# Kernel optimization log

Hardware: AMD Instinct MI355X
Metric: run time of the kernel (lower is better)

## Reference

```python
import jax, jax.numpy as jnp
import numpy as np

D_MODEL = 2048
NUM_HEADS = 16
D_FF = 8192
BATCH = 4
SEQ = 2048


def setup_inputs() -> dict:
    key = jax.random.key(0)
    ks = jax.random.split(key, 16)
    s_attn = 1.0 / np.sqrt(D_MODEL)
    s_ff1 = 1.0 / np.sqrt(D_MODEL)
    s_ff2 = 1.0 / np.sqrt(D_FF)
    return {
        "x": jax.random.normal(ks[0], (BATCH, SEQ, D_MODEL), dtype=jnp.float32),
        "Wq": jax.random.normal(ks[1], (D_MODEL, D_MODEL), dtype=jnp.float32) * s_attn,
        "bq": jnp.zeros((D_MODEL,), dtype=jnp.float32),
        "Wk": jax.random.normal(ks[2], (D_MODEL, D_MODEL), dtype=jnp.float32) * s_attn,
        "bk": jnp.zeros((D_MODEL,), dtype=jnp.float32),
        "Wv": jax.random.normal(ks[3], (D_MODEL, D_MODEL), dtype=jnp.float32) * s_attn,
        "bv": jnp.zeros((D_MODEL,), dtype=jnp.float32),
        "Wo": jax.random.normal(ks[4], (D_MODEL, D_MODEL), dtype=jnp.float32) * s_attn,
        "bo": jnp.zeros((D_MODEL,), dtype=jnp.float32),
        "W1": jax.random.normal(ks[5], (D_MODEL, D_FF), dtype=jnp.float32) * s_ff1,
        "b1": jnp.zeros((D_FF,), dtype=jnp.float32),
        "W2": jax.random.normal(ks[6], (D_FF, D_MODEL), dtype=jnp.float32) * s_ff2,
        "b2": jnp.zeros((D_MODEL,), dtype=jnp.float32),
        "ln1_g": jnp.ones((D_MODEL,), dtype=jnp.float32),
        "ln1_b": jnp.zeros((D_MODEL,), dtype=jnp.float32),
        "ln2_g": jnp.ones((D_MODEL,), dtype=jnp.float32),
        "ln2_b": jnp.zeros((D_MODEL,), dtype=jnp.float32),
    }


def _layer_norm(x, g, b, eps=1e-5):
    mu = jnp.mean(x, axis=-1, keepdims=True)
    var = jnp.mean(jnp.square(x - mu), axis=-1, keepdims=True)
    return (x - mu) * jax.lax.rsqrt(var + eps) * g + b


def _attention(h, Wq, bq, Wk, bk, Wv, bv, Wo, bo):
    B, S, D = h.shape
    H = NUM_HEADS
    dk = D // H
    q = (h @ Wq + bq).reshape(B, S, H, dk).transpose(0, 2, 1, 3)  # bhsd
    k = (h @ Wk + bk).reshape(B, S, H, dk).transpose(0, 2, 1, 3)
    v = (h @ Wv + bv).reshape(B, S, H, dk).transpose(0, 2, 1, 3)
    logits = jnp.einsum("bhqd,bhkd->bhqk", q, k) / jnp.sqrt(jnp.float32(dk))
    causal = jnp.triu(jnp.ones((S, S), dtype=bool), k=1)  # True above diagonal
    logits = jnp.where(causal, -jnp.inf, logits)
    attn = jax.nn.softmax(logits, axis=-1)
    out = jnp.einsum("bhqk,bhkd->bhqd", attn, v)
    out = out.transpose(0, 2, 1, 3).reshape(B, S, D)
    return out @ Wo + bo


def reference(x, Wq, bq, Wk, bk, Wv, bv, Wo, bo, W1, b1, W2, b2,
              ln1_g, ln1_b, ln2_g, ln2_b):
    # Pre-LN attention block + residual
    h = _layer_norm(x, ln1_g, ln1_b)
    x = x + _attention(h, Wq, bq, Wk, bk, Wv, bv, Wo, bo)
    # Pre-LN FFN block + residual (GELU activation)
    h = _layer_norm(x, ln2_g, ln2_b)
    ff = jax.nn.gelu(h @ W1 + b1, approximate=False) @ W2 + b2
    return x + ff
```

## Files before the change

kernel.cpp:

```cpp
#include <hip/hip_runtime.h>
#include <hip/hip_bf16.h>

#define D_MODEL 2048
#define NUM_HEADS 16
#define D_FF 8192
#define BATCH 4
#define SEQ 2048
#define DK 128
#define MTOT (BATCH * SEQ)

typedef __attribute__((ext_vector_type(8))) short short8;
typedef __attribute__((ext_vector_type(4))) short short4v;
typedef __attribute__((ext_vector_type(4))) float f32x4;

#define MFMA16(a, b, c) __builtin_amdgcn_mfma_f32_16x16x32_bf16(a, b, c, 0, 0, 0)

#define GLOAD16(gp, lp)                                                        \
  __builtin_amdgcn_global_load_lds(                                            \
      (const __attribute__((address_space(1))) void*)(gp),                     \
      (__attribute__((address_space(3))) void*)(lp), 16, 0, 0)

static __device__ __forceinline__ unsigned short f2bf(float f) {
  return __builtin_bit_cast(unsigned short, __float2bfloat16(f));
}

__global__ __launch_bounds__(256) void transpose_cvt_kernel(
    const float* __restrict__ in, __hip_bfloat16* __restrict__ out, int K, int N) {
  __shared__ float tile[32][33];
  const int n0 = blockIdx.x * 32, k0 = blockIdx.y * 32;
  const int tx = threadIdx.x & 31, ty = threadIdx.x >> 5;
#pragma unroll
  for (int i = 0; i < 4; ++i)
    tile[ty + i * 8][tx] = in[(size_t)(k0 + ty + i * 8) * N + n0 + tx];
  __syncthreads();
#pragma unroll
  for (int i = 0; i < 4; ++i)
    out[(size_t)(n0 + ty + i * 8) * K + k0 + tx] = __float2bfloat16(tile[tx][ty + i * 8]);
}

__global__ __launch_bounds__(256) void layernorm_kernel(
    const float* __restrict__ x, const float* __restrict__ g,
    const float* __restrict__ bta, __hip_bfloat16* __restrict__ out) {
  const int row = blockIdx.x;
  const int tid = threadIdx.x;
  const float* xr = x + (size_t)row * D_MODEL;
  float4 v0 = *(const float4*)(xr + tid * 8);
  float4 v1 = *(const float4*)(xr + tid * 8 + 4);
  float s = v0.x + v0.y + v0.z + v0.w + v1.x + v1.y + v1.z + v1.w;
  float q = v0.x * v0.x + v0.y * v0.y + v0.z * v0.z + v0.w * v0.w +
            v1.x * v1.x + v1.y * v1.y + v1.z * v1.z + v1.w * v1.w;
#pragma unroll
  for (int off = 1; off < 64; off <<= 1) {
    s += __shfl_xor(s, off);
    q += __shfl_xor(q, off);
  }
  __shared__ float rs[4], rq[4];
  if ((tid & 63) == 0) {
    rs[tid >> 6] = s;
    rq[tid >> 6] = q;
  }
  __syncthreads();
  s = rs[0] + rs[1] + rs[2] + rs[3];
  q = rq[0] + rq[1] + rq[2] + rq[3];
  const float mu = s * (1.0f / D_MODEL);
  const float var = q * (1.0f / D_MODEL) - mu * mu;
  const float rstd = rsqrtf(var + 1e-5f);
  float4 g0 = *(const float4*)(g + tid * 8);
  float4 g1 = *(const float4*)(g + tid * 8 + 4);
  float4 b0 = *(const float4*)(bta + tid * 8);
  float4 b1 = *(const float4*)(bta + tid * 8 + 4);
  short8 o;
  o[0] = (short)f2bf((v0.x - mu) * rstd * g0.x + b0.x);
  o[1] = (short)f2bf((v0.y - mu) * rstd * g0.y + b0.y);
  o[2] = (short)f2bf((v0.z - mu) * rstd * g0.z + b0.z);
  o[3] = (short)f2bf((v0.w - mu) * rstd * g0.w + b0.w);
  o[4] = (short)f2bf((v1.x - mu) * rstd * g1.x + b1.x);
  o[5] = (short)f2bf((v1.y - mu) * rstd * g1.y + b1.y);
  o[6] = (short)f2bf((v1.z - mu) * rstd * g1.z + b1.z);
  o[7] = (short)f2bf((v1.w - mu) * rstd * g1.w + b1.w);
  *(short8*)(out + (size_t)row * D_MODEL + tid * 8) = o;
}

enum { EPI_BF16 = 0, EPI_VT = 1, EPI_RESID = 2, EPI_GELU = 3 };

template <int EPI>
__global__ __launch_bounds__(256, 2) void gemm_kernel(
    const __hip_bfloat16* __restrict__ A, const __hip_bfloat16* __restrict__ Bt,
    const float* __restrict__ bias, const float* __restrict__ resid,
    void* __restrict__ outv, int M, int N, int K) {
  __shared__ __align__(16) unsigned char sA[16384];
  __shared__ __align__(16) unsigned char sB[16384];
  const int tid = threadIdx.x;
  const int lane = tid & 63, w = tid >> 6;
  const int l15 = lane & 15, lg = lane >> 4;
  const int m0 = blockIdx.y * 128, n0 = blockIdx.x * 128;
  const int wm = (w >> 1) * 64, wn = (w & 1) * 64;

  f32x4 acc[4][4] = {};

  const int row8 = lane >> 3;
  const int g8 = (lane & 7) ^ row8;

  for (int kt = 0; kt < K; kt += 64) {
#pragma unroll
    for (int i = 0; i < 4; ++i) {
      const int c = w * 4 + i;
      const int row = c * 8 + row8;
      GLOAD16(A + (size_t)(m0 + row) * K + kt + g8 * 8, sA + c * 1024);
      GLOAD16(Bt + (size_t)(n0 + row) * K + kt + g8 * 8, sB + c * 1024);
    }
    __syncthreads();
#pragma unroll
    for (int ks = 0; ks < 2; ++ks) {
      const int cb = ks * 4 + lg;
      short8 af[4], bf[4];
#pragma unroll
      for (int f = 0; f < 4; ++f) {
        const int ra = wm + f * 16 + l15;
        af[f] = *(const short8*)(sA + ra * 128 + ((cb ^ (ra & 7)) << 4));
        const int rb = wn + f * 16 + l15;
        bf[f] = *(const short8*)(sB + rb * 128 + ((cb ^ (rb & 7)) << 4));
      }
#pragma unroll
      for (int fi = 0; fi < 4; ++fi)
#pragma unroll
        for (int fj = 0; fj < 4; ++fj)
          acc[fi][fj] = MFMA16(af[fi], bf[fj], acc[fi][fj]);
    }
    __syncthreads();
  }

#pragma unroll
  for (int fi = 0; fi < 4; ++fi) {
#pragma unroll
    for (int fj = 0; fj < 4; ++fj) {
      const int mb = m0 + wm + fi * 16 + lg * 4;
      const int n = n0 + wn + fj * 16 + l15;
      const float bv = bias ? bias[n] : 0.0f;
      if constexpr (EPI == EPI_VT) {
        const int bb = mb >> 11, ss = mb & (SEQ - 1);
        const int hh = n >> 7, dd = n & (DK - 1);
        short4v pk;
#pragma unroll
        for (int r = 0; r < 4; ++r) pk[r] = (short)f2bf(acc[fi][fj][r] + bv);
        __hip_bfloat16* o = (__hip_bfloat16*)outv;
        *(short4v*)(o + ((size_t)((bb * NUM_HEADS + hh) * DK + dd)) * SEQ + ss) = pk;
      } else {
#pragma unroll
        for (int r = 0; r < 4; ++r) {
          const int m = mb + r;
          const float v = acc[fi][fj][r] + bv;
          if constexpr (EPI == EPI_BF16) {
            ((__hip_bfloat16*)outv)[(size_t)m * N + n] = __float2bfloat16(v);
          } else if constexpr (EPI == EPI_GELU) {
            const float ge = 0.5f * v * (1.0f + erff(v * 0.70710678118654752f));
            ((__hip_bfloat16*)outv)[(size_t)m * N + n] = __float2bfloat16(ge);
          } else {
            ((float*)outv)[(size_t)m * N + n] = resid[(size_t)m * N + n] + v;
          }
        }
      }
    }
  }
}

__global__ __launch_bounds__(512, 4) void attn_kernel(
    const __hip_bfloat16* __restrict__ Qm, const __hip_bfloat16* __restrict__ Km,
    const __hip_bfloat16* __restrict__ Vt, __hip_bfloat16* __restrict__ Om) {
  __shared__ __align__(16) unsigned char Kl[2][16384];
  __shared__ __align__(16) unsigned char Vl[2][16384];
  __shared__ __align__(16) unsigned char Pl[16384];
  const int tid = threadIdx.x;
  const int lane = tid & 63, w = tid >> 6;
  const int l15 = lane & 15, lg = lane >> 4;
  const int bh = blockIdx.y, b = bh >> 4, h = bh & 15;
  const int q0 = blockIdx.x * 128;
  const int qw = q0 + w * 16;
  const int row8 = lane >> 3;
  const int nt = (q0 >> 6) + 2;

  short8 qf[4];
  const __hip_bfloat16* qbase = Qm + (size_t)(b * SEQ + qw + l15) * D_MODEL + h * DK;
#pragma unroll
  for (int ks = 0; ks < 4; ++ks) qf[ks] = *(const short8*)(qbase + ks * 32 + lg * 8);

  float m_run[4], l_run[4];
  f32x4 acc_o[8];
#pragma unroll
  for (int r = 0; r < 4; ++r) { m_run[r] = -1e30f; l_run[r] = 0.0f; }
#pragma unroll
  for (int fd = 0; fd < 8; ++fd) acc_o[fd] = (f32x4){0.f, 0.f, 0.f, 0.f};

  auto STAGE = [&](int tt) {
    unsigned char* kb = Kl[tt & 1];
    unsigned char* vb = Vl[tt & 1];
    const int t0 = tt * 64;
#pragma unroll
    for (int i = 0; i < 2; ++i) {
      const int c = w * 2 + i;
      const int row = c * 4 + lg;
      const int gcb = l15 ^ (row & 7);
      GLOAD16(Km + (size_t)(b * SEQ + t0 + row) * D_MODEL + h * DK + gcb * 8,
              kb + c * 1024);
    }
#pragma unroll
    for (int i = 0; i < 2; ++i) {
      const int c = w * 2 + i;
      const int row = c * 8 + row8;
      const int gcb = (lane & 7) ^ (row & 7);
      GLOAD16(Vt + (size_t)(bh * DK + row) * SEQ + t0 + gcb * 8, vb + c * 1024);
    }
  };

  STAGE(0);
  for (int t = 0; t < nt; ++t) {
    const int t0 = t * 64;
    if (t + 1 < nt) {
      STAGE(t + 1);
      asm volatile("s_waitcnt vmcnt(4)" ::: "memory");
    } else {
      asm volatile("s_waitcnt vmcnt(0)" ::: "memory");
    }
    __builtin_amdgcn_s_barrier();
    asm volatile("" ::: "memory");
    if (t0 <= qw + 15) {
      const unsigned char* kb = Kl[t & 1];
      const unsigned char* vb = Vl[t & 1];
      f32x4 sacc[4];
#pragma unroll
      for (int fn = 0; fn < 4; ++fn) sacc[fn] = (f32x4){0.f, 0.f, 0.f, 0.f};
#pragma unroll
      for (int ks = 0; ks < 4; ++ks) {
        const int cb = ks * 4 + lg;
#pragma unroll
        for (int fn = 0; fn < 4; ++fn) {
          const int rn = fn * 16 + l15;
          short8 kf = *(const short8*)(kb + rn * 256 + ((cb ^ (rn & 7)) << 4));
          sacc[fn] = MFMA16(qf[ks], kf, sacc[fn]);
        }
      }
      const float scale = 0.088388347648318447f;
      float mt[4] = {-1e30f, -1e30f, -1e30f, -1e30f};
#pragma unroll
      for (int fn = 0; fn < 4; ++fn) {
        const int key = t0 + fn * 16 + l15;
#pragma unroll
        for (int r = 0; r < 4; ++r) {
          const int qg = qw + lg * 4 + r;
          float sv = sacc[fn][r] * scale;
          sv = (key <= qg) ? sv : -1e30f;
          sacc[fn][r] = sv;
          mt[r] = fmaxf(mt[r], sv);
        }
      }
      float alpha[4], ls[4];
#pragma unroll
      for (int r = 0; r < 4; ++r) {
#pragma unroll
        for (int off = 1; off < 16; off <<= 1) mt[r] = fmaxf(mt[r], __shfl_xor(mt[r], off));
        const float mnew = fmaxf(m_run[r], mt[r]);
        alpha[r] = __expf(m_run[r] - mnew);
        m_run[r] = mnew;
        ls[r] = 0.0f;
      }
#pragma unroll
      for (int fn = 0; fn < 4; ++fn)
#pragma unroll
        for (int r = 0; r < 4; ++r) {
          const float p = __expf(sacc[fn][r] - m_run[r]);
          sacc[fn][r] = p;
          ls[r] += p;
        }
#pragma unroll
      for (int r = 0; r < 4; ++r) {
#pragma unroll
        for (int off = 1; off < 16; off <<= 1) ls[r] += __shfl_xor(ls[r], off);
        l_run[r] = l_run[r] * alpha[r] + ls[r];
      }
#pragma unroll
      for (int fd = 0; fd < 8; ++fd)
#pragma unroll
        for (int r = 0; r < 4; ++r) acc_o[fd][r] *= alpha[r];
      unsigned char* pw = Pl + w * 2048;
#pragma unroll
      for (int fn = 0; fn < 4; ++fn) {
        const int tt = fn * 16 + l15;
#pragma unroll
        for (int r = 0; r < 4; ++r) {
          const int qq = lg * 4 + r;
          *(unsigned short*)(pw + qq * 128 + (((tt >> 3) ^ (qq & 7)) << 4) +
                             (tt & 7) * 2) = f2bf(sacc[fn][r]);
        }
      }
#pragma unroll
      for (int ks = 0; ks < 2; ++ks) {
#pragma unroll
        for (int half = 0; half < 2; ++half) {
          const int tb = (ks * 2 + half) * 2 + (lg & 1) + (lg >> 1) * 0;
        }
        const int tb = ks * 4 + lg;
        short8 pf = *(const short8*)(Pl + w * 2048 + l15 * 128 +
                                     ((tb ^ (l15 & 7)) << 4));
        const int cb = ks * 4 + lg;
#pragma unroll
        for (int fd = 0; fd < 8; ++fd) {
          const int rv = fd * 16 + l15;
          short8 vf = *(const short8*)(vb + rv * 128 + ((cb ^ (rv & 7)) << 4));
          acc_o[fd] = MFMA16(pf, vf, acc_o[fd]);
        }
      }
    }
    asm volatile("" ::: "memory");
    __builtin_amdgcn_s_barrier();
    asm volatile("" ::: "memory");
  }
#pragma unroll
  for (int r = 0; r < 4; ++r) {
    const float inv = 1.0f / l_run[r];
    const int qg = qw + lg * 4 + r;
    __hip_bfloat16* ob = Om + (size_t)(b * SEQ + qg) * D_MODEL + h * DK + l15;
#pragma unroll
    for (int fd = 0; fd < 8; ++fd)
      ob[fd * 16] = __float2bfloat16(acc_o[fd][r] * inv);
  }
}

extern "C" void kernel_launch(void* const* d_in, const int* in_sizes, int n_in,
                              void* d_out, int out_size, void* d_ws, size_t ws_size,
                              hipStream_t stream) {
  (void)in_sizes; (void)n_in; (void)out_size;
  const size_t MB = 1024 * 1024;
  if (ws_size < 192 * MB) return;

  const float* x  = (const float*)d_in[0];
  const float* Wq = (const float*)d_in[1];
  const float* bq = (const float*)d_in[2];
  const float* Wk = (const float*)d_in[3];
  const float* bk = (const float*)d_in[4];
  const float* Wv = (const float*)d_in[5];
  const float* bv = (const float*)d_in[6];
  const float* Wo = (const float*)d_in[7];
  const float* bo = (const float*)d_in[8];
  const float* W1 = (const float*)d_in[9];
  const float* b1 = (const float*)d_in[10];
  const float* W2 = (const float*)d_in[11];
  const float* b2 = (const float*)d_in[12];
  const float* g1 = (const float*)d_in[13];
  const float* be1 = (const float*)d_in[14];
  const float* g2 = (const float*)d_in[15];
  const float* be2 = (const float*)d_in[16];

  char* ws = (char*)d_ws;
  __hip_bfloat16* Hb  = (__hip_bfloat16*)(ws + 0 * MB);
  __hip_bfloat16* Qb  = (__hip_bfloat16*)(ws + 32 * MB);
  __hip_bfloat16* Kb  = (__hip_bfloat16*)(ws + 64 * MB);
  __hip_bfloat16* Vtb = (__hip_bfloat16*)(ws + 96 * MB);
  __hip_bfloat16* AOb = (__hip_bfloat16*)(ws + 128 * MB);
  __hip_bfloat16* W1T = (__hip_bfloat16*)(ws + 32 * MB);
  __hip_bfloat16* W2T = (__hip_bfloat16*)(ws + 64 * MB);
  __hip_bfloat16* FF1 = (__hip_bfloat16*)(ws + 96 * MB);
  __hip_bfloat16* WqT = (__hip_bfloat16*)(ws + 160 * MB);
  __hip_bfloat16* WkT = (__hip_bfloat16*)(ws + 168 * MB);
  __hip_bfloat16* WvT = (__hip_bfloat16*)(ws + 176 * MB);
  __hip_bfloat16* WoT = (__hip_bfloat16*)(ws + 184 * MB);
  float* X2 = (float*)d_out;

  const dim3 tb(256);
  transpose_cvt_kernel<<<dim3(64, 64), tb, 0, stream>>>(Wq, WqT, 2048, 2048);
  transpose_cvt_kernel<<<dim3(64, 64), tb, 0, stream>>>(Wk, WkT, 2048, 2048);
  transpose_cvt_kernel<<<dim3(64, 64), tb, 0, stream>>>(Wv, WvT, 2048, 2048);
  transpose_cvt_kernel<<<dim3(64, 64), tb, 0, stream>>>(Wo, WoT, 2048, 2048);

  layernorm_kernel<<<MTOT, tb, 0, stream>>>(x, g1, be1, Hb);

  const dim3 gQKV(2048 / 128, MTOT / 128);
  gemm_kernel<EPI_BF16><<<gQKV, tb, 0, stream>>>(Hb, WqT, bq, nullptr, Qb, MTOT, 2048, 2048);
  gemm_kernel<EPI_BF16><<<gQKV, tb, 0, stream>>>(Hb, WkT, bk, nullptr, Kb, MTOT, 2048, 2048);
  gemm_kernel<EPI_VT><<<gQKV, tb, 0, stream>>>(Hb, WvT, bv, nullptr, Vtb, MTOT, 2048, 2048);

  attn_kernel<<<dim3(SEQ / 128, BATCH * NUM_HEADS), dim3(512), 0, stream>>>(Qb, Kb, Vtb, AOb);

  transpose_cvt_kernel<<<dim3(256, 64), tb, 0, stream>>>(W1, W1T, 2048, 8192);
  transpose_cvt_kernel<<<dim3(64, 256), tb, 0, stream>>>(W2, W2T, 8192, 2048);

  gemm_kernel<EPI_RESID><<<gQKV, tb, 0, stream>>>(AOb, WoT, bo, x, X2, MTOT, 2048, 2048);

  layernorm_kernel<<<MTOT, tb, 0, stream>>>(X2, g2, be2, Hb);

  for (int c = 0; c < 2; ++c) {
    const size_t moff = (size_t)c * 4096;
    gemm_kernel<EPI_GELU><<<dim3(8192 / 128, 4096 / 128), tb, 0, stream>>>(
        Hb + moff * D_MODEL, W1T, b1, nullptr, FF1, 4096, 8192, 2048);
    gemm_kernel<EPI_RESID><<<dim3(2048 / 128, 4096 / 128), tb, 0, stream>>>(
        FF1, W2T, b2, X2 + moff * D_MODEL, X2 + moff * D_MODEL, 4096, 2048, 8192);
  }
}
```

Baseline: 1.376 ms.

## Triple-buffer GEMM K-loop with 256x128 tiles and 512-thread blocks

The bf16 GEMM moves from a 128x128 tile with 256 threads and two barriers per K-step to a 256x128 tile with 8 waves. It now uses a three-stage LDS ring filled by global_load_lds, issued two K-steps ahead and gated by vmcnt waits and one barrier per step. MFMA blocks are wrapped in s_setprio to favour the math waves. The goal is to hide global-load latency behind MFMA work and to raise data reuse per block. The cost is 144KB of LDS per block, which limits occupancy to one block per CU, and fewer blocks for the smaller GEMMs.

After: 1.348 ms. -2.0%, faster.

```diff
diff --git a/kernel.cpp b/kernel.cpp
--- a/kernel.cpp
+++ b/kernel.cpp
@@ -84,16 +84,15 @@
 enum { EPI_BF16 = 0, EPI_VT = 1, EPI_RESID = 2, EPI_GELU = 3 };
 
 template <int EPI>
-__global__ __launch_bounds__(256, 2) void gemm_kernel(
+__global__ __launch_bounds__(512, 2) void gemm_kernel(
     const __hip_bfloat16* __restrict__ A, const __hip_bfloat16* __restrict__ Bt,
     const float* __restrict__ bias, const float* __restrict__ resid,
     void* __restrict__ outv, int M, int N, int K) {
-  __shared__ __align__(16) unsigned char sA[16384];
-  __shared__ __align__(16) unsigned char sB[16384];
+  __shared__ __align__(16) unsigned char lds[3][49152];
   const int tid = threadIdx.x;
   const int lane = tid & 63, w = tid >> 6;
   const int l15 = lane & 15, lg = lane >> 4;
-  const int m0 = blockIdx.y * 128, n0 = blockIdx.x * 128;
+  const int m0 = blockIdx.y * 256, n0 = blockIdx.x * 128;
   const int wm = (w >> 1) * 64, wn = (w & 1) * 64;
 
   f32x4 acc[4][4] = {};
@@ -101,15 +100,24 @@
   const int row8 = lane >> 3;
   const int g8 = (lane & 7) ^ row8;
 
-  for (int kt = 0; kt < K; kt += 64) {
+  auto STAGE = [&](int tt) {
+    unsigned char* db = lds[tt % 3];
+    const size_t ko = (size_t)tt * 64;
 #pragma unroll
     for (int i = 0; i < 4; ++i) {
       const int c = w * 4 + i;
       const int row = c * 8 + row8;
-      GLOAD16(A + (size_t)(m0 + row) * K + kt + g8 * 8, sA + c * 1024);
-      GLOAD16(Bt + (size_t)(n0 + row) * K + kt + g8 * 8, sB + c * 1024);
-    }
-    __syncthreads();
+      GLOAD16(A + (size_t)(m0 + row) * K + ko + g8 * 8, db + c * 1024);
+    }
+#pragma unroll
+    for (int i = 0; i < 2; ++i) {
+      const int c = w * 2 + i;
+      const int row = c * 8 + row8;
+      GLOAD16(Bt + (size_t)(n0 + row) * K + ko + g8 * 8, db + 32768 + c * 1024);
+    }
+  };
+  auto COMPUTE = [&](int tt) {
+    const unsigned char* db = lds[tt % 3];
 #pragma unroll
     for (int ks = 0; ks < 2; ++ks) {
       const int cb = ks * 4 + lg;
@@ -117,17 +125,36 @@
 #pragma unroll
       for (int f = 0; f < 4; ++f) {
         const int ra = wm + f * 16 + l15;
-        af[f] = *(const short8*)(sA + ra * 128 + ((cb ^ (ra & 7)) << 4));
+        af[f] = *(const short8*)(db + ra * 128 + ((cb ^ (ra & 7)) << 4));
         const int rb = wn + f * 16 + l15;
-        bf[f] = *(const short8*)(sB + rb * 128 + ((cb ^ (rb & 7)) << 4));
-      }
+        bf[f] = *(const short8*)(db + 32768 + rb * 128 + ((cb ^ (rb & 7)) << 4));
+      }
+      __builtin_amdgcn_s_setprio(1);
 #pragma unroll
       for (int fi = 0; fi < 4; ++fi)
 #pragma unroll
         for (int fj = 0; fj < 4; ++fj)
           acc[fi][fj] = MFMA16(af[fi], bf[fj], acc[fi][fj]);
-    }
-    __syncthreads();
+      __builtin_amdgcn_s_setprio(0);
+    }
+  };
+
+  const int nt = K >> 6;
+  STAGE(0);
+  STAGE(1);
+  for (int t = 0; t < nt; ++t) {
+    if (t + 2 < nt) {
+      asm volatile("s_waitcnt vmcnt(6)" ::: "memory");
+      __builtin_amdgcn_s_barrier();
+      STAGE(t + 2);
+    } else if (t + 2 == nt) {
+      asm volatile("s_waitcnt vmcnt(6)" ::: "memory");
+      __builtin_amdgcn_s_barrier();
+    } else {
+      asm volatile("s_waitcnt vmcnt(0)" ::: "memory");
+      __builtin_amdgcn_s_barrier();
+    }
+    COMPUTE(t);
   }
 
 #pragma unroll
@@ -294,10 +321,6 @@
       }
 #pragma unroll
       for (int ks = 0; ks < 2; ++ks) {
-#pragma unroll
-        for (int half = 0; half < 2; ++half) {
-          const int tb = (ks * 2 + half) * 2 + (lg & 1) + (lg >> 1) * 0;
-        }
         const int tb = ks * 4 + lg;
         short8 pf = *(const short8*)(Pl + w * 2048 + l15 * 128 +
                                      ((tb ^ (l15 & 7)) << 4));
@@ -373,25 +396,25 @@
 
   layernorm_kernel<<<MTOT, tb, 0, stream>>>(x, g1, be1, Hb);
 
-  const dim3 gQKV(2048 / 128, MTOT / 128);
-  gemm_kernel<EPI_BF16><<<gQKV, tb, 0, stream>>>(Hb, WqT, bq, nullptr, Qb, MTOT, 2048, 2048);
-  gemm_kernel<EPI_BF16><<<gQKV, tb, 0, stream>>>(Hb, WkT, bk, nullptr, Kb, MTOT, 2048, 2048);
-  gemm_kernel<EPI_VT><<<gQKV, tb, 0, stream>>>(Hb, WvT, bv, nullptr, Vtb, MTOT, 2048, 2048);
+  const dim3 gQKV(2048 / 128, MTOT / 256);
+  gemm_kernel<EPI_BF16><<<gQKV, 512, 0, stream>>>(Hb, WqT, bq, nullptr, Qb, MTOT, 2048, 2048);
+  gemm_kernel<EPI_BF16><<<gQKV, 512, 0, stream>>>(Hb, WkT, bk, nullptr, Kb, MTOT, 2048, 2048);
+  gemm_kernel<EPI_VT><<<gQKV, 512, 0, stream>>>(Hb, WvT, bv, nullptr, Vtb, MTOT, 2048, 2048);
 
   attn_kernel<<<dim3(SEQ / 128, BATCH * NUM_HEADS), dim3(512), 0, stream>>>(Qb, Kb, Vtb, AOb);
 
   transpose_cvt_kernel<<<dim3(256, 64), tb, 0, stream>>>(W1, W1T, 2048, 8192);
   transpose_cvt_kernel<<<dim3(64, 256), tb, 0, stream>>>(W2, W2T, 8192, 2048);
 
-  gemm_kernel<EPI_RESID><<<gQKV, tb, 0, stream>>>(AOb, WoT, bo, x, X2, MTOT, 2048, 2048);
+  gemm_kernel<EPI_RESID><<<gQKV, 512, 0, stream>>>(AOb, WoT, bo, x, X2, MTOT, 2048, 2048);
 
   layernorm_kernel<<<MTOT, tb, 0, stream>>>(X2, g2, be2, Hb);
 
   for (int c = 0; c < 2; ++c) {
     const size_t moff = (size_t)c * 4096;
-    gemm_kernel<EPI_GELU><<<dim3(8192 / 128, 4096 / 128), tb, 0, stream>>>(
+    gemm_kernel<EPI_GELU><<<dim3(8192 / 128, 4096 / 256), 512, 0, stream>>>(
         Hb + moff * D_MODEL, W1T, b1, nullptr, FF1, 4096, 8192, 2048);
-    gemm_kernel<EPI_RESID><<<dim3(2048 / 128, 4096 / 128), tb, 0, stream>>>(
+    gemm_kernel<EPI_RESID><<<dim3(2048 / 128, 4096 / 256), 512, 0, stream>>>(
         FF1, W2T, b2, X2 + moff * D_MODEL, X2 + moff * D_MODEL, 4096, 2048, 8192);
   }
 }
```
